# Kernel optimization log

Measured on AMD Instinct MI355X. Metric: run time of the kernel, lower is better.

## Reference

```python
import jax, jax.numpy as jnp
import numpy as np

B, C = 32, 2048

def setup_inputs() -> dict:
    key = jax.random.key(0)
    k1, k2, k3 = jax.random.split(key, 3)
    x1 = jax.random.normal(k1, (B, C), dtype=jnp.float32)
    x2 = jax.random.normal(k2, (B, C), dtype=jnp.float32)
    # 1x1 conv over 2C->C channels on a 1x1 spatial map == dense layer (C, 2C)
    W = jax.random.normal(k3, (C, 2 * C), dtype=jnp.float32) * (1.0 / np.sqrt(2 * C))
    b = jnp.zeros((C,), dtype=jnp.float32)
    return {"x1": x1, "x2": x2, "W": W, "b": b}


def reference(x1, x2, W, b):
    # conv1x1 fusion of the two (B,C) inputs -> (B,C)
    x = jnp.concatenate([x1, x2], axis=1) @ W.T + b  # (B, C)
    # energy[b,i,j] = x[b,i] * x[b,j]  (H*W == 1 -> rank-1 outer product)
    energy = x[:, :, None] * x[:, None, :]  # (B, C, C)
    # max-subtraction variant: softmax(max_j(energy) - energy) along last dim
    energy_new = jnp.max(energy, axis=-1, keepdims=True) - energy
    attention = jax.nn.softmax(energy_new, axis=-1)  # (B, C, C)
    # attention @ value (value is (B,C,1) since H=W=1) -> matvec, then residual
    out1 = jnp.einsum('bij,bj->bi', attention, x1) + x1  # (B, C)
    out2 = jnp.einsum('bij,bj->bi', attention, x2) + x2  # (B, C)
    return out1, out2, attention
```

## Files before the change

### kernel.cpp

```cpp
#include <hip/hip_runtime.h>

#define CDIM 2048
#define BATCH 32
#define K2 4096

typedef float f32x4 __attribute__((ext_vector_type(4)));

#define BN 64
#define BK 128
#define KT (K2 / BK)
#define NT (CDIM / BN)

__global__ __launch_bounds__(256) void gemm_partial_k(
    const float* __restrict__ x1, const float* __restrict__ x2,
    const float* __restrict__ W, float* __restrict__ partial)
{
    __shared__ float Xs[BATCH][BK + 1];
    __shared__ float Wt[BN][BK + 1];
    const int nt = blockIdx.x, kt = blockIdx.y;
    const int i0 = nt * BN, k0 = kt * BK;
    const int t = threadIdx.x;

    const float* xsrc = (k0 < CDIM) ? x1 : x2;
    const int kk0 = k0 & (CDIM - 1);

    #pragma unroll
    for (int r = 0; r < 4; ++r) {
        int f = t + 256 * r;
        int b = f >> 5, c4 = (f & 31) * 4;
        float4 v = *reinterpret_cast<const float4*>(xsrc + b * CDIM + kk0 + c4);
        Xs[b][c4 + 0] = v.x; Xs[b][c4 + 1] = v.y;
        Xs[b][c4 + 2] = v.z; Xs[b][c4 + 3] = v.w;
    }
    #pragma unroll
    for (int r = 0; r < 8; ++r) {
        int f = t + 256 * r;
        int row = f >> 5, c4 = (f & 31) * 4;
        float4 v = *reinterpret_cast<const float4*>(W + (size_t)(i0 + row) * K2 + k0 + c4);
        Wt[row][c4 + 0] = v.x; Wt[row][c4 + 1] = v.y;
        Wt[row][c4 + 2] = v.z; Wt[row][c4 + 3] = v.w;
    }
    __syncthreads();

    const int j = t & 31, bg = t >> 5;
    const int il = j * 2, b0 = bg * 4;
    float acc[4][2] = {};
    #pragma unroll 4
    for (int kk = 0; kk < BK; ++kk) {
        float w0 = Wt[il][kk], w1 = Wt[il + 1][kk];
        #pragma unroll
        for (int bb = 0; bb < 4; ++bb) {
            float xv = Xs[b0 + bb][kk];
            acc[bb][0] = fmaf(xv, w0, acc[bb][0]);
            acc[bb][1] = fmaf(xv, w1, acc[bb][1]);
        }
    }
    #pragma unroll
    for (int bb = 0; bb < 4; ++bb) {
        float2 v = make_float2(acc[bb][0], acc[bb][1]);
        *reinterpret_cast<float2*>(partial + (size_t)kt * (BATCH * CDIM)
                                   + (b0 + bb) * CDIM + i0 + il) = v;
    }
}

__global__ __launch_bounds__(256) void reduce_x_k(
    const float* __restrict__ partial, const float* __restrict__ bias,
    float* __restrict__ x)
{
    int idx = blockIdx.x * 256 + threadIdx.x;
    float s = 0.f;
    #pragma unroll
    for (int kt = 0; kt < KT; ++kt) s += partial[(size_t)kt * (BATCH * CDIM) + idx];
    x[idx] = s + bias[idx & (CDIM - 1)];
}

__global__ __launch_bounds__(256) void attn_k(
    const float* __restrict__ x, const float* __restrict__ x1,
    const float* __restrict__ x2, float* __restrict__ out1,
    float* __restrict__ out2, float* __restrict__ att)
{
    __shared__ float xs[CDIM];
    __shared__ float xs1[CDIM];
    __shared__ float xs2[CDIM];
    __shared__ float wred[8];
    const int b = blockIdx.x >> 5, rg = blockIdx.x & 31;
    const int t = threadIdx.x;
    const int lane = t & 63, wv = t >> 6;
    const float* xb  = x  + b * CDIM;
    const float* x1b = x1 + b * CDIM;
    const float* x2b = x2 + b * CDIM;

    #pragma unroll
    for (int r = 0; r < 2; ++r) {
        int f = (t + 256 * r) * 4;
        *reinterpret_cast<float4*>(&xs[f])  = *reinterpret_cast<const float4*>(xb  + f);
        *reinterpret_cast<float4*>(&xs1[f]) = *reinterpret_cast<const float4*>(x1b + f);
        *reinterpret_cast<float4*>(&xs2[f]) = *reinterpret_cast<const float4*>(x2b + f);
    }
    __syncthreads();

    float mn = 1e30f, mx = -1e30f;
    for (int f = t; f < CDIM; f += 256) {
        float v = xs[f];
        mn = fminf(mn, v); mx = fmaxf(mx, v);
    }
    #pragma unroll
    for (int off = 32; off > 0; off >>= 1) {
        mn = fminf(mn, __shfl_xor(mn, off));
        mx = fmaxf(mx, __shfl_xor(mx, off));
    }
    if (lane == 0) { wred[wv] = mn; wred[4 + wv] = mx; }
    __syncthreads();
    mn = fminf(fminf(wred[0], wred[1]), fminf(wred[2], wred[3]));
    mx = fmaxf(fmaxf(wred[4], wred[5]), fmaxf(wred[6], wred[7]));

    for (int r = 0; r < 16; ++r) {
        const int i = rg * 64 + wv * 16 + r;
        const float xi = xs[i];
        const float li = (xi >= 0.f) ? xi * mn : xi * mx;
        const float nxi = -xi;
        float sum = 0.f, d1 = 0.f, d2 = 0.f;
        #pragma unroll
        for (int g = 0; g < 8; ++g) {
            const int o = g * 256 + lane * 4;
            f32x4 xv = *reinterpret_cast<const f32x4*>(&xs[o]);
            f32x4 v1 = *reinterpret_cast<const f32x4*>(&xs1[o]);
            f32x4 v2 = *reinterpret_cast<const f32x4*>(&xs2[o]);
            #pragma unroll
            for (int c = 0; c < 4; ++c) {
                float ev = __expf(fmaf(nxi, xv[c], li));
                sum += ev;
                d1 = fmaf(ev, v1[c], d1);
                d2 = fmaf(ev, v2[c], d2);
            }
        }
        #pragma unroll
        for (int off = 32; off > 0; off >>= 1) {
            sum += __shfl_xor(sum, off);
            d1  += __shfl_xor(d1, off);
            d2  += __shfl_xor(d2, off);
        }
        const float inv = 1.f / sum;
        if (lane == 0) {
            out1[b * CDIM + i] = fmaf(d1, inv, xs1[i]);
            out2[b * CDIM + i] = fmaf(d2, inv, xs2[i]);
        }
        float* arow = att + (size_t)(b * CDIM + i) * CDIM;
        #pragma unroll
        for (int g = 0; g < 8; ++g) {
            const int o = g * 256 + lane * 4;
            f32x4 xv = *reinterpret_cast<const f32x4*>(&xs[o]);
            f32x4 v;
            #pragma unroll
            for (int c = 0; c < 4; ++c)
                v[c] = __expf(fmaf(nxi, xv[c], li)) * inv;
            *reinterpret_cast<f32x4*>(arow + o) = v;
        }
    }
}

extern "C" void kernel_launch(void* const* d_in, const int* in_sizes, int n_in,
                              void* d_out, int out_size, void* d_ws, size_t ws_size,
                              hipStream_t stream) {
    const float* x1   = (const float*)d_in[0];
    const float* x2   = (const float*)d_in[1];
    const float* W    = (const float*)d_in[2];
    const float* bias = (const float*)d_in[3];
    float* out  = (float*)d_out;
    float* out1 = out;
    float* out2 = out + BATCH * CDIM;
    float* att  = out + 2 * BATCH * CDIM;
    float* x    = (float*)d_ws;

    float* partial = out + ((size_t)out_size - (size_t)KT * BATCH * CDIM);

    gemm_partial_k<<<dim3(NT, KT), dim3(256), 0, stream>>>(x1, x2, W, partial);
    reduce_x_k<<<(BATCH * CDIM) / 256, 256, 0, stream>>>(partial, bias, x);
    attn_k<<<BATCH * (CDIM / 64), 256, 0, stream>>>(x, x1, x2, out1, out2, att);
}
```

Before: 126.2 us.

## Restructure GEMM partial kernel with register tiling, XOR-swizzled LDS and intra-block K split

The shared-memory tiles become flat arrays written with float4 stores and an XOR swizzle in place of padding, which is meant to avoid bank conflicts on vector reads. Each thread now computes a 4x8 output tile from float4 LDS loads, and the block's four wavefronts each take a quarter of the K range. The four partial accumulators are then reduced through LDS and written out as float4 stores. This cuts LDS traffic per FMA and widens global stores, at the cost of more registers and an extra LDS reduction step. The GEMM stage is likely a small part of total time, since the attention kernel writes a 512 MB output.

Result: faster. 123.0 us (-2.5%).

```diff
diff --git a/kernel.cpp b/kernel.cpp
--- a/kernel.cpp
+++ b/kernel.cpp
@@ -15,51 +15,84 @@
     const float* __restrict__ x1, const float* __restrict__ x2,
     const float* __restrict__ W, float* __restrict__ partial)
 {
-    __shared__ float Xs[BATCH][BK + 1];
-    __shared__ float Wt[BN][BK + 1];
+    __shared__ float lds[BN * BK + BATCH * BK];
+    float* Wt = lds;
+    float* Xs = lds + BN * BK;
+
     const int nt = blockIdx.x, kt = blockIdx.y;
     const int i0 = nt * BN, k0 = kt * BK;
     const int t = threadIdx.x;
+    const int lane = t & 63, ks = t >> 6;
+    const int cg = lane & 7, bg = lane >> 3;
 
     const float* xsrc = (k0 < CDIM) ? x1 : x2;
     const int kk0 = k0 & (CDIM - 1);
 
     #pragma unroll
+    for (int r = 0; r < 8; ++r) {
+        int f = t + 256 * r;
+        int row = f >> 5, kc = f & 31;
+        float4 v = *reinterpret_cast<const float4*>(W + (size_t)(i0 + row) * K2 + k0 + kc * 4);
+        int sc = kc ^ ((row >> 3) & 7);
+        *reinterpret_cast<float4*>(&Wt[row * BK + sc * 4]) = v;
+    }
+    #pragma unroll
     for (int r = 0; r < 4; ++r) {
         int f = t + 256 * r;
-        int b = f >> 5, c4 = (f & 31) * 4;
-        float4 v = *reinterpret_cast<const float4*>(xsrc + b * CDIM + kk0 + c4);
-        Xs[b][c4 + 0] = v.x; Xs[b][c4 + 1] = v.y;
-        Xs[b][c4 + 2] = v.z; Xs[b][c4 + 3] = v.w;
-    }
-    #pragma unroll
-    for (int r = 0; r < 8; ++r) {
-        int f = t + 256 * r;
-        int row = f >> 5, c4 = (f & 31) * 4;
-        float4 v = *reinterpret_cast<const float4*>(W + (size_t)(i0 + row) * K2 + k0 + c4);
-        Wt[row][c4 + 0] = v.x; Wt[row][c4 + 1] = v.y;
-        Wt[row][c4 + 2] = v.z; Wt[row][c4 + 3] = v.w;
-    }
-    __syncthreads();
-
-    const int j = t & 31, bg = t >> 5;
-    const int il = j * 2, b0 = bg * 4;
-    float acc[4][2] = {};
-    #pragma unroll 4
-    for (int kk = 0; kk < BK; ++kk) {
-        float w0 = Wt[il][kk], w1 = Wt[il + 1][kk];
-        #pragma unroll
-        for (int bb = 0; bb < 4; ++bb) {
-            float xv = Xs[b0 + bb][kk];
-            acc[bb][0] = fmaf(xv, w0, acc[bb][0]);
-            acc[bb][1] = fmaf(xv, w1, acc[bb][1]);
-        }
-    }
-    #pragma unroll
-    for (int bb = 0; bb < 4; ++bb) {
-        float2 v = make_float2(acc[bb][0], acc[bb][1]);
-        *reinterpret_cast<float2*>(partial + (size_t)kt * (BATCH * CDIM)
-                                   + (b0 + bb) * CDIM + i0 + il) = v;
+        int row = f >> 5, kc = f & 31;
+        float4 v = *reinterpret_cast<const float4*>(xsrc + row * CDIM + kk0 + kc * 4);
+        int sc = kc ^ ((row >> 2) & 7);
+        *reinterpret_cast<float4*>(&Xs[row * BK + sc * 4]) = v;
+    }
+    __syncthreads();
+
+    float acc[4][8] = {};
+    #pragma unroll 2
+    for (int s = 0; s < 8; ++s) {
+        const int kc = ks * 8 + s;
+        f32x4 xv[4], wv[8];
+        #pragma unroll
+        for (int bb = 0; bb < 4; ++bb)
+            xv[bb] = *reinterpret_cast<const f32x4*>(&Xs[(4 * bg + bb) * BK + (kc ^ bg) * 4]);
+        #pragma unroll
+        for (int cc = 0; cc < 8; ++cc)
+            wv[cc] = *reinterpret_cast<const f32x4*>(&Wt[(8 * cg + cc) * BK + (kc ^ cg) * 4]);
+        #pragma unroll
+        for (int bb = 0; bb < 4; ++bb)
+            #pragma unroll
+            for (int cc = 0; cc < 8; ++cc)
+                #pragma unroll
+                for (int w = 0; w < 4; ++w)
+                    acc[bb][cc] = fmaf(xv[bb][w], wv[cc][w], acc[bb][cc]);
+    }
+
+    __syncthreads();
+    float* accS = lds;
+    #pragma unroll
+    for (int bb = 0; bb < 4; ++bb)
+        #pragma unroll
+        for (int cc = 0; cc < 8; ++cc)
+            accS[(ks * 64 + lane) * 33 + bb * 8 + cc] = acc[bb][cc];
+    __syncthreads();
+
+    {
+        const int l0 = t >> 2, q = t & 3;
+        float s0[8];
+        #pragma unroll
+        for (int j = 0; j < 8; ++j) {
+            float s = 0.f;
+            #pragma unroll
+            for (int k = 0; k < 4; ++k)
+                s += accS[(k * 64 + l0) * 33 + q * 8 + j];
+            s0[j] = s;
+        }
+        const int b_row = 4 * (l0 >> 3) + q;
+        const int icol  = 8 * (l0 & 7);
+        float* dst = partial + (size_t)kt * (BATCH * CDIM) + b_row * CDIM + i0 + icol;
+        float4 lo = make_float4(s0[0], s0[1], s0[2], s0[3]);
+        float4 hi = make_float4(s0[4], s0[5], s0[6], s0[7]);
+        *reinterpret_cast<float4*>(dst)     = lo;
+        *reinterpret_cast<float4*>(dst + 4) = hi;
     }
 }
 
```
